# Performance work log

Hardware: AMD Instinct MI355X
Metric: run time of the kernel (lower is better)

The kernel has to match this reference:

```python
import jax, jax.numpy as jnp
import numpy as np

NUM_CLASSES = 21


def setup_inputs() -> dict:
    key = jax.random.key(0)
    k1, k2 = jax.random.split(key)
    B, C, H, W = 8, NUM_CLASSES, 512, 512
    inputs = jax.random.normal(k1, (B, C, H, W), dtype=jnp.float32)
    targets = jax.random.randint(k2, (B, H, W), 0, C, dtype=jnp.int64)
    return {"inputs": inputs, "targets": targets}


def reference(inputs, targets):
    # inputs: [B, C, H, W] logits; targets: [B, H, W] int labels
    B, C, H, W = inputs.shape
    # Hard predictions are detached in the original (Variable(inputs.data...))
    predicts = jax.lax.stop_gradient(jnp.argmax(inputs, axis=1))  # [B, H, W]
    probs = jax.nn.softmax(inputs, axis=1)                        # [B, C, H, W]

    classes = jnp.arange(C)
    # Per-class binary masks, vectorized over C.
    # Note: the original's i==0 branch (invert nonzero/zero) reduces to the
    # same (x == i) indicator as the i>0 branch.
    pm = predicts[:, None, :, :] == classes[None, :, None, None]  # [B, C, H, W] bool
    tm = targets[:, None, :, :] == classes[None, :, None, None]   # [B, C, H, W] bool
    union_mask = (pm | tm).astype(probs.dtype)      # union with 2 -> 1 clamp
    intersect_mask = (pm & tm).astype(probs.dtype)

    # Soft-weighted per-class sums over batch-flattened spatial dims.
    union = jnp.sum(probs * union_mask, axis=(2, 3))        # [B, C]
    intersect = jnp.sum(probs * intersect_mask, axis=(2, 3))  # [B, C]

    ratio = intersect / jnp.maximum(union, 1.0)  # [B, C]
    # Per class: MSELoss(ratio, 1) = mean over batch; then sum over classes.
    iou_loss = jnp.sum(jnp.mean((ratio - 1.0) ** 2, axis=0))
    return iou_loss
```

## Files before the change

kernel.cpp:

```cpp
#include <hip/hip_runtime.h>

#define NCLS 21
#define HW (512 * 512)
#define NP (HW / 2)
#define BATCH 8
#define BLOCK 256
#define GRIDX (NP / BLOCK)

#define WS_FLOATS (2 * BATCH * NCLS)

__global__ void zero_ws_kernel(float* ws) {
    int i = blockIdx.x * blockDim.x + threadIdx.x;
    if (i < WS_FLOATS) ws[i] = 0.0f;
}

__global__ __launch_bounds__(BLOCK) void iou_partial_kernel(
        const float* __restrict__ in,
        const int* __restrict__ tgt,
        float* __restrict__ ws) {
    const int b = blockIdx.y;
    const float2* __restrict__ in2 = (const float2*)(in + (size_t)b * NCLS * HW);
    const int2*   __restrict__ tb2 = (const int2*)(tgt + (size_t)b * HW);

    __shared__ float s_u[NCLS];
    __shared__ float s_i[NCLS];
    if (threadIdx.x < NCLS) { s_u[threadIdx.x] = 0.0f; s_i[threadIdx.x] = 0.0f; }
    __syncthreads();

    const int p = blockIdx.x * BLOCK + threadIdx.x;

    const int2 t2 = tb2[p];
    float2 x[NCLS];
    #pragma unroll
    for (int c = 0; c < NCLS; ++c)
        x[c] = in2[(size_t)c * NP + p];

    const int t[2] = {t2.x, t2.y};
    #pragma unroll
    for (int j = 0; j < 2; ++j) {
        const int tj = t[j];
        float m  = (j == 0) ? x[0].x : x[0].y;
        int   aj = 0;
        #pragma unroll
        for (int c = 1; c < NCLS; ++c) {
            const float v = (j == 0) ? x[c].x : x[c].y;
            const bool g = v > m;
            aj = g ? c : aj;
            m  = g ? v : m;
        }
        float s  = 0.0f;
        float et = 0.0f;
        #pragma unroll
        for (int c = 0; c < NCLS; ++c) {
            const float v = (j == 0) ? x[c].x : x[c].y;
            const float e = __expf(v - m);
            s += e;
            et = (c == tj) ? e : et;
        }
        const float p_pred = 1.0f / s;
        const float p_t    = et * p_pred;
        const bool  eq = (tj == aj);
        atomicAdd(&s_u[aj], p_pred);
        atomicAdd(eq ? &s_i[aj] : &s_u[tj], eq ? p_pred : p_t);
    }

    __syncthreads();
    if (threadIdx.x < NCLS) {
        atomicAdd(&ws[b * NCLS + threadIdx.x], s_u[threadIdx.x]);
        atomicAdd(&ws[BATCH * NCLS + b * NCLS + threadIdx.x], s_i[threadIdx.x]);
    }
}

__global__ __launch_bounds__(BLOCK) void finalize_kernel(
        const float* __restrict__ ws, float* __restrict__ out) {
    __shared__ float red[BLOCK];
    const int i = threadIdx.x;
    float val = 0.0f;
    if (i < BATCH * NCLS) {
        const float u  = ws[i];
        const float it = ws[BATCH * NCLS + i];
        const float ratio = it / fmaxf(u, 1.0f);
        const float d = ratio - 1.0f;
        val = d * d;
    }
    red[i] = val;
    __syncthreads();
    for (int off = BLOCK / 2; off > 0; off >>= 1) {
        if (i < off) red[i] += red[i + off];
        __syncthreads();
    }
    if (i == 0) out[0] = red[0] / (float)BATCH;
}

extern "C" void kernel_launch(void* const* d_in, const int* in_sizes, int n_in,
                              void* d_out, int out_size, void* d_ws, size_t ws_size,
                              hipStream_t stream) {
    const float* in  = (const float*)d_in[0];
    const int*   tgt = (const int*)d_in[1];
    float* ws  = (float*)d_ws;
    float* out = (float*)d_out;

    zero_ws_kernel<<<1, 512, 0, stream>>>(ws);
    dim3 grid(GRIDX, BATCH);
    iou_partial_kernel<<<grid, BLOCK, 0, stream>>>(in, tgt, ws);
    finalize_kernel<<<1, BLOCK, 0, stream>>>(ws, out);
}
```

Before: 249.1 us.

## Vectorize to float4 loads, process more pixels per thread, drop global atomics

Each thread now loads float4 logits and int4 targets and handles two quads, i.e. eight pixels, so the grid shrinks from 512 to 128 blocks per image. Global atomicAdd accumulation is replaced by per-block partial sums written to the workspace, which the finalize kernel then reduces. This removes the zero-init kernel launch and atomic contention. In exchange each thread holds many more registers (21 float4 values per iteration), which may reduce occupancy, and the finalize kernel now does a serial reduction over 128 partials per (b, c).

After: 254.9 us. 2.3% more time.

```diff
diff --git a/kernel.cpp b/kernel.cpp
--- a/kernel.cpp
+++ b/kernel.cpp
@@ -2,90 +2,106 @@
 
 #define NCLS 21
 #define HW (512 * 512)
-#define NP (HW / 2)
+#define QP (HW / 4)
 #define BATCH 8
 #define BLOCK 256
-#define GRIDX (NP / BLOCK)
+#define QPT 2
+#define BPI (QP / (BLOCK * QPT))
+#define NB (BATCH * BPI)
 
-#define WS_FLOATS (2 * BATCH * NCLS)
 
-__global__ void zero_ws_kernel(float* ws) {
-    int i = blockIdx.x * blockDim.x + threadIdx.x;
-    if (i < WS_FLOATS) ws[i] = 0.0f;
+__device__ __forceinline__ float comp(const float4& v, int j) {
+    return j == 0 ? v.x : j == 1 ? v.y : j == 2 ? v.z : v.w;
 }
 
 __global__ __launch_bounds__(BLOCK) void iou_partial_kernel(
         const float* __restrict__ in,
-        const int* __restrict__ tgt,
+        const int*   __restrict__ tgt,
         float* __restrict__ ws) {
-    const int b = blockIdx.y;
-    const float2* __restrict__ in2 = (const float2*)(in + (size_t)b * NCLS * HW);
-    const int2*   __restrict__ tb2 = (const int2*)(tgt + (size_t)b * HW);
+    const int b   = blockIdx.y;
+    const int blk = blockIdx.x;
+    const float4* __restrict__ in4 = (const float4*)(in + (size_t)b * NCLS * HW);
+    const int4*   __restrict__ tg4 = (const int4*)(tgt + (size_t)b * HW);
 
     __shared__ float s_u[NCLS];
     __shared__ float s_i[NCLS];
     if (threadIdx.x < NCLS) { s_u[threadIdx.x] = 0.0f; s_i[threadIdx.x] = 0.0f; }
     __syncthreads();
 
-    const int p = blockIdx.x * BLOCK + threadIdx.x;
+    #pragma unroll
+    for (int it = 0; it < QPT; ++it) {
+        const int q = (blk * QPT + it) * BLOCK + threadIdx.x;
+        const int4 t4 = tg4[q];
+        float4 x[NCLS];
+        #pragma unroll
+        for (int c = 0; c < NCLS; ++c)
+            x[c] = in4[(size_t)c * QP + q];
 
-    const int2 t2 = tb2[p];
-    float2 x[NCLS];
-    #pragma unroll
-    for (int c = 0; c < NCLS; ++c)
-        x[c] = in2[(size_t)c * NP + p];
-
-    const int t[2] = {t2.x, t2.y};
-    #pragma unroll
-    for (int j = 0; j < 2; ++j) {
-        const int tj = t[j];
-        float m  = (j == 0) ? x[0].x : x[0].y;
-        int   aj = 0;
+        const int tj4[4] = {t4.x, t4.y, t4.z, t4.w};
         #pragma unroll
-        for (int c = 1; c < NCLS; ++c) {
-            const float v = (j == 0) ? x[c].x : x[c].y;
-            const bool g = v > m;
-            aj = g ? c : aj;
-            m  = g ? v : m;
+        for (int j = 0; j < 4; ++j) {
+            const int tj = tj4[j];
+            float m  = comp(x[0], j);
+            int   aj = 0;
+            #pragma unroll
+            for (int c = 1; c < NCLS; ++c) {
+                const float v = comp(x[c], j);
+                const bool g = v > m;
+                aj = g ? c : aj;
+                m  = g ? v : m;
+            }
+            float s  = 0.0f;
+            float et = 0.0f;
+            #pragma unroll
+            for (int c = 0; c < NCLS; ++c) {
+                const float v = comp(x[c], j);
+                const float e = __expf(v - m);
+                s += e;
+                et = (c == tj) ? e : et;
+            }
+            const float p_pred = 1.0f / s;
+            const float p_t    = et * p_pred;
+            const bool  eq = (tj == aj);
+            atomicAdd(&s_u[aj], p_pred);
+            atomicAdd(eq ? &s_i[aj] : &s_u[tj], eq ? p_pred : p_t);
         }
-        float s  = 0.0f;
-        float et = 0.0f;
-        #pragma unroll
-        for (int c = 0; c < NCLS; ++c) {
-            const float v = (j == 0) ? x[c].x : x[c].y;
-            const float e = __expf(v - m);
-            s += e;
-            et = (c == tj) ? e : et;
-        }
-        const float p_pred = 1.0f / s;
-        const float p_t    = et * p_pred;
-        const bool  eq = (tj == aj);
-        atomicAdd(&s_u[aj], p_pred);
-        atomicAdd(eq ? &s_i[aj] : &s_u[tj], eq ? p_pred : p_t);
     }
 
     __syncthreads();
-    if (threadIdx.x < NCLS) {
-        atomicAdd(&ws[b * NCLS + threadIdx.x], s_u[threadIdx.x]);
-        atomicAdd(&ws[BATCH * NCLS + b * NCLS + threadIdx.x], s_i[threadIdx.x]);
+    if (threadIdx.x < 2 * NCLS) {
+        const float v = (threadIdx.x < NCLS) ? s_u[threadIdx.x]
+                                             : s_i[threadIdx.x - NCLS];
+        ws[(size_t)threadIdx.x * NB + b * BPI + blk] = v;
     }
 }
 
-__global__ __launch_bounds__(BLOCK) void finalize_kernel(
+__global__ __launch_bounds__(256) void finalize_kernel(
         const float* __restrict__ ws, float* __restrict__ out) {
-    __shared__ float red[BLOCK];
+    __shared__ float red[256];
     const int i = threadIdx.x;
     float val = 0.0f;
     if (i < BATCH * NCLS) {
-        const float u  = ws[i];
-        const float it = ws[BATCH * NCLS + i];
-        const float ratio = it / fmaxf(u, 1.0f);
-        const float d = ratio - 1.0f;
-        val = d * d;
+        const int b = i / NCLS;
+        const int c = i % NCLS;
+        const float4* __restrict__ u4 =
+            (const float4*)(ws + (size_t)c * NB + b * BPI);
+        const float4* __restrict__ i4 =
+            (const float4*)(ws + (size_t)(NCLS + c) * NB + b * BPI);
+        float u = 0.0f, t = 0.0f;
+        #pragma unroll 8
+        for (int k = 0; k < BPI / 4; ++k) {
+            const float4 a = u4[k];
+            u += a.x + a.y + a.z + a.w;
+            const float4 d = i4[k];
+            t += d.x + d.y + d.z + d.w;
+        }
+        const float ratio = t / fmaxf(u, 1.0f);
+        const float dd = ratio - 1.0f;
+        val = dd * dd;
     }
     red[i] = val;
     __syncthreads();
-    for (int off = BLOCK / 2; off > 0; off >>= 1) {
+    for (int off = 128; off > 0; off >>= 1) {
         if (i < off) red[i] += red[i + off];
         __syncthreads();
     }
@@ -100,8 +116,7 @@
     float* ws  = (float*)d_ws;
     float* out = (float*)d_out;
 
-    zero_ws_kernel<<<1, 512, 0, stream>>>(ws);
-    dim3 grid(GRIDX, BATCH);
+    dim3 grid(BPI, BATCH);
     iou_partial_kernel<<<grid, BLOCK, 0, stream>>>(in, tgt, ws);
-    finalize_kernel<<<1, BLOCK, 0, stream>>>(ws, out);
+    finalize_kernel<<<1, 256, 0, stream>>>(ws, out);
 }
```
